# Performance work log

Hardware: AMD Instinct MI355X
Metric: run time of the kernel (lower is better)

The kernel has to match this reference:

```python
import jax, jax.numpy as jnp
import numpy as np

B, T, C, H = 4, 2048, 1024, 16
D = C // H  # head dim = 64


def setup_inputs() -> dict:
    key = jax.random.key(0)
    ks = jax.random.split(key, 6)
    s = 1.0 / np.sqrt(C)
    return {
        "x": jax.random.normal(ks[0], (B, T, C), dtype=jnp.float32),
        "Wk": jax.random.uniform(ks[1], (C, C), jnp.float32, -s, s),
        "Wq": jax.random.uniform(ks[2], (C, C), jnp.float32, -s, s),
        "Wv": jax.random.uniform(ks[3], (C, C), jnp.float32, -s, s),
        "Wp": jax.random.uniform(ks[4], (C, C), jnp.float32, -s, s),
        "bp": jax.random.uniform(ks[5], (C,), jnp.float32, -s, s),
    }


def reference(x, Wk, Wq, Wv, Wp, bp):
    # nn.Linear applies y = x @ W.T
    def split_heads(y):  # [B,T,C] -> [B,H,T,D]
        return y.reshape(B, T, H, D).transpose(0, 2, 1, 3)

    k = split_heads(x @ Wk.T)
    q = split_heads(x @ Wq.T)
    v = split_heads(x @ Wv.T)
    scale = 1.0 / np.sqrt(D)
    aff = jnp.einsum("bhtd,bhsd->bhts", q, k) * scale  # [B,H,T,T]
    aff = jax.nn.softmax(aff, axis=-1)
    out = jnp.einsum("bhts,bhsd->bhtd", aff, v)  # [B,H,T,D]
    out = out.transpose(0, 2, 1, 3).reshape(B, T, C)
    return out @ Wp.T + bp
```

## Files before the change

kernel.cpp:

```cpp
#include <hip/hip_runtime.h>
#include <stdint.h>

typedef __bf16 bf16_t;
typedef bf16_t bf16x2 __attribute__((ext_vector_type(2)));
typedef bf16_t bf16x8 __attribute__((ext_vector_type(8)));
typedef float f32x4 __attribute__((ext_vector_type(4)));
typedef float f32x16 __attribute__((ext_vector_type(16)));
typedef unsigned short u16;
typedef u16 u16x8 __attribute__((ext_vector_type(8)));
typedef u16 u16x4 __attribute__((ext_vector_type(4)));
typedef unsigned int u32;
typedef u32 u32x2 __attribute__((ext_vector_type(2)));
typedef u32 u32x4v __attribute__((ext_vector_type(4)));

__device__ __forceinline__ u16 f2b(float f) {
  uint32_t u = __builtin_bit_cast(uint32_t, f);
  u += 0x7fffu + ((u >> 16) & 1u);
  return (u16)(u >> 16);
}

__device__ __forceinline__ u32 pkbf(float lo, float hi) {
  bf16x2 t = {(__bf16)lo, (__bf16)hi};
  return __builtin_bit_cast(u32, t);
}

__device__ __forceinline__ void gl_lds16(const void* g, void* l) {
  __builtin_amdgcn_global_load_lds(
      (const __attribute__((address_space(1))) uint32_t*)(uintptr_t)g,
      (__attribute__((address_space(3))) uint32_t*)(uintptr_t)l, 16, 0, 0);
}

__global__ void cast_bf16(const float* __restrict__ src, u16* __restrict__ dst, int n8) {
  int i = blockIdx.x * blockDim.x + threadIdx.x;
  int stride = gridDim.x * blockDim.x;
  for (; i < n8; i += stride) {
    float4 a = ((const float4*)src)[2 * i];
    float4 b = ((const float4*)src)[2 * i + 1];
    u16x8 o;
    o[0] = f2b(a.x); o[1] = f2b(a.y); o[2] = f2b(a.z); o[3] = f2b(a.w);
    o[4] = f2b(b.x); o[5] = f2b(b.y); o[6] = f2b(b.z); o[7] = f2b(b.w);
    ((u16x8*)dst)[i] = o;
  }
}

__global__ void cast4_bf16(const float* __restrict__ a, const float* __restrict__ b,
                           const float* __restrict__ c, const float* __restrict__ d,
                           u16* __restrict__ dst, int n8) {
  const float* srcs[4] = {a, b, c, d};
  const float* src = srcs[blockIdx.y];
  u16* dp = dst + (size_t)blockIdx.y * (size_t)n8 * 8;
  int i = blockIdx.x * blockDim.x + threadIdx.x;
  int stride = gridDim.x * blockDim.x;
  for (; i < n8; i += stride) {
    float4 x = ((const float4*)src)[2 * i];
    float4 y = ((const float4*)src)[2 * i + 1];
    u16x8 o;
    o[0] = f2b(x.x); o[1] = f2b(x.y); o[2] = f2b(x.z); o[3] = f2b(x.w);
    o[4] = f2b(y.x); o[5] = f2b(y.y); o[6] = f2b(y.z); o[7] = f2b(y.w);
    ((u16x8*)dp)[i] = o;
  }
}

template <int MODE>
__global__ __launch_bounds__(256, 2)
void gemm_bt(const u16* __restrict__ A, const u16* __restrict__ Wt,
             u16* __restrict__ outb, float* __restrict__ outf,
             const float* __restrict__ bias, float scale) {
  __shared__ u16 As[128 * 32];
  __shared__ u16 Bs[128 * 32];
  const int tid  = threadIdx.x;
  const int lane = tid & 63;
  const int w    = tid >> 6;
  const int wm   = w >> 1, wn = w & 1;
  const int g    = lane >> 4, c = lane & 15;
  const int m0   = blockIdx.y * 128, n0 = blockIdx.x * 128;

  f32x4 acc[4][4] = {};

  const u16* gA = A  + (size_t)(m0 + w * 16 + (lane >> 2)) * 1024 + (lane & 3) * 8;
  const u16* gB = Wt + (size_t)(n0 + w * 16 + (lane >> 2)) * 1024 + (lane & 3) * 8;
  char* lA = (char*)As + w * 1024;
  char* lB = (char*)Bs + w * 1024;

#pragma unroll 1
  for (int kt = 0; kt < 1024; kt += 32) {
    __syncthreads();
    gl_lds16(gA + kt,             lA);
    gl_lds16(gA + kt + 64 * 1024, lA + 4096);
    gl_lds16(gB + kt,             lB);
    gl_lds16(gB + kt + 64 * 1024, lB + 4096);
    __syncthreads();
    bf16x8 af[4], bfr[4];
#pragma unroll
    for (int mi = 0; mi < 4; ++mi)
      af[mi] = *(const bf16x8*)&As[(wm * 64 + mi * 16 + c) * 32 + g * 8];
#pragma unroll
    for (int ni = 0; ni < 4; ++ni)
      bfr[ni] = *(const bf16x8*)&Bs[(wn * 64 + ni * 16 + c) * 32 + g * 8];
#pragma unroll
    for (int mi = 0; mi < 4; ++mi)
#pragma unroll
      for (int ni = 0; ni < 4; ++ni)
        acc[mi][ni] = __builtin_amdgcn_mfma_f32_16x16x32_bf16(af[mi], bfr[ni], acc[mi][ni], 0, 0, 0);
  }

  const int rowb = m0 + wm * 64;
  const int colb = n0 + wn * 64;

  if (MODE == 0) {
#pragma unroll
    for (int mi = 0; mi < 4; ++mi)
#pragma unroll
      for (int ni = 0; ni < 4; ++ni) {
        size_t base = (size_t)(rowb + mi * 16 + g * 4) * 1024 + (colb + ni * 16 + c);
#pragma unroll
        for (int r = 0; r < 4; ++r)
          outb[base + (size_t)r * 1024] = f2b(acc[mi][ni][r] * scale);
      }
  } else if (MODE == 1) {
#pragma unroll
    for (int mi = 0; mi < 4; ++mi) {
      int row = rowb + mi * 16 + g * 4;
      int bb = row >> 11, tl = row & 2047;
#pragma unroll
      for (int ni = 0; ni < 4; ++ni) {
        int col = colb + ni * 16 + c;
        u16x4 pk;
#pragma unroll
        for (int r = 0; r < 4; ++r) pk[r] = f2b(acc[mi][ni][r]);
        *(u16x4*)(outb + ((size_t)(bb * 1024 + col)) * 2048 + tl) = pk;
      }
    }
  } else {
#pragma unroll
    for (int ni = 0; ni < 4; ++ni) {
      int col = colb + ni * 16 + c;
      float bv = bias[col];
#pragma unroll
      for (int mi = 0; mi < 4; ++mi) {
        size_t base = (size_t)(rowb + mi * 16 + g * 4) * 1024 + col;
#pragma unroll
        for (int r = 0; r < 4; ++r)
          outf[base + (size_t)r * 1024] = acc[mi][ni][r] + bv;
      }
    }
  }
}

__global__ __launch_bounds__(256, 2)
void attn_fused(const u16* __restrict__ qb, const u16* __restrict__ kb,
                const u16* __restrict__ vt, u16* __restrict__ ob) {
  __shared__ u16 KV[2][4096];

  const int bh = blockIdx.x;
  const int qt = blockIdx.y;
  const int b  = bh >> 4, h = bh & 15;
  const int tid  = threadIdx.x;
  const int lane = tid & 63;
  const int w    = tid >> 6;
  const int l31  = lane & 31, g32 = lane >> 5;

  const int r  = tid >> 3, sl = tid & 7;
  const u16* kgp = kb + (size_t)(b * 2048 + r) * 1024 + h * 64 + sl * 8;
  const u16* vgp = vt + (size_t)(bh * 64 + r) * 2048 + sl * 8;
  const int wb = r * 128 + ((sl * 16) ^ ((r & 7) << 4));
  char* lK = (char*)&KV[0][0];
  char* lV = (char*)&KV[1][0];

  const int qrow0 = b * 2048 + qt * 256 + w * 64;
  bf16x8 qf[2][4];
#pragma unroll
  for (int q2 = 0; q2 < 2; ++q2)
#pragma unroll
    for (int dc = 0; dc < 4; ++dc)
      qf[q2][dc] = *(const bf16x8*)(qb + (size_t)(qrow0 + q2 * 32 + l31) * 1024 +
                                    h * 64 + dc * 16 + g32 * 8);

  f32x16 Oa[2][2] = {};
  float lp[2] = {0.f, 0.f};

  const int xorv = (l31 & 7) << 4;
  const int rowb = l31 * 128;

  uint4 pK0 = *(const uint4*)(kgp);
  uint4 pK1 = *(const uint4*)(kgp + (size_t)32 * 1024);
  uint4 pV0 = *(const uint4*)(vgp);
  uint4 pV1 = *(const uint4*)(vgp + (size_t)32 * 2048);

#pragma unroll 1
  for (int step = 0; step < 32; ++step) {
    __syncthreads();
    *(uint4*)(lK + wb)        = pK0;
    *(uint4*)(lK + wb + 4096) = pK1;
    *(uint4*)(lV + wb)        = pV0;
    *(uint4*)(lV + wb + 4096) = pV1;
    __syncthreads();

    if (step + 1 < 32) {
      const int s1 = (step + 1) * 64;
      pK0 = *(const uint4*)(kgp + (size_t)s1 * 1024);
      pK1 = *(const uint4*)(kgp + (size_t)(s1 + 32) * 1024);
      pV0 = *(const uint4*)(vgp + s1);
      pV1 = *(const uint4*)(vgp + s1 + (size_t)32 * 2048);
    }

    const char* kt  = (const char*)&KV[0][0];
    const char* vtl = (const char*)&KV[1][0];

#pragma unroll
    for (int kb2 = 0; kb2 < 2; ++kb2) {
      bf16x8 kf[4];
#pragma unroll
      for (int dc = 0; dc < 4; ++dc)
        kf[dc] = *(const bf16x8*)(kt + kb2 * 4096 + rowb + ((dc * 32 + g32 * 16) ^ xorv));
      bf16x8 vf[2][2];
#pragma unroll
      for (int db = 0; db < 2; ++db)
#pragma unroll
        for (int ck = 0; ck < 2; ++ck)
          vf[db][ck] = *(const bf16x8*)(vtl + db * 4096 + rowb +
                                        (((kb2 * 2 + ck) * 32 + g32 * 16) ^ xorv));

#pragma unroll
      for (int q2 = 0; q2 < 2; ++q2) {
        f32x16 S = {};
#pragma unroll
        for (int dc = 0; dc < 4; ++dc)
          S = __builtin_amdgcn_mfma_f32_32x32x16_bf16(kf[dc], qf[q2][dc], S, 0, 0, 0);

        float p[16];
#pragma unroll
        for (int rr = 0; rr < 16; ++rr) p[rr] = __builtin_amdgcn_exp2f(S[rr]);
        float s01 = (p[0] + p[1]) + (p[2] + p[3]);
        float s02 = (p[4] + p[5]) + (p[6] + p[7]);
        float s03 = (p[8] + p[9]) + (p[10] + p[11]);
        float s04 = (p[12] + p[13]) + (p[14] + p[15]);
        lp[q2] += (s01 + s02) + (s03 + s04);

        u32 w0 = pkbf(p[0], p[1]),   w1 = pkbf(p[2], p[3]);
        u32 w2 = pkbf(p[4], p[5]),   w3 = pkbf(p[6], p[7]);
        u32 w4 = pkbf(p[8], p[9]),   w5 = pkbf(p[10], p[11]);
        u32 w6 = pkbf(p[12], p[13]), w7 = pkbf(p[14], p[15]);
        u32x2 sA = __builtin_amdgcn_permlane32_swap(w0, w2, false, false);
        u32x2 sB = __builtin_amdgcn_permlane32_swap(w1, w3, false, false);
        u32x2 sC = __builtin_amdgcn_permlane32_swap(w4, w6, false, false);
        u32x2 sD = __builtin_amdgcn_permlane32_swap(w5, w7, false, false);
        u32x4v q0 = {sA[0], sB[0], sA[1], sB[1]};
        u32x4v q1 = {sC[0], sD[0], sC[1], sD[1]};
        bf16x8 pb0 = __builtin_bit_cast(bf16x8, q0);
        bf16x8 pb1 = __builtin_bit_cast(bf16x8, q1);

#pragma unroll
        for (int db = 0; db < 2; ++db) {
          Oa[q2][db] = __builtin_amdgcn_mfma_f32_32x32x16_bf16(vf[db][0], pb0, Oa[q2][db], 0, 0, 0);
          Oa[q2][db] = __builtin_amdgcn_mfma_f32_32x32x16_bf16(vf[db][1], pb1, Oa[q2][db], 0, 0, 0);
        }
      }
    }
  }

#pragma unroll
  for (int q2 = 0; q2 < 2; ++q2) {
    float v = lp[q2];
    v += __shfl_xor(v, 32);
    float rinv = 1.0f / v;
    const size_t rb = (size_t)(qrow0 + q2 * 32 + l31) * 1024 + h * 64;
#pragma unroll
    for (int db = 0; db < 2; ++db)
#pragma unroll
      for (int pr = 0; pr < 8; ++pr) {
        int reg = 2 * pr;
        int d0  = (reg & 3) + 8 * (reg >> 2) + 4 * g32 + db * 32;
        u32 pk = pkbf(Oa[q2][db][reg] * rinv, Oa[q2][db][reg + 1] * rinv);
        *(u32*)(ob + rb + d0) = pk;
      }
  }
}

extern "C" void kernel_launch(void* const* d_in, const int* in_sizes, int n_in,
                              void* d_out, int out_size, void* d_ws, size_t ws_size,
                              hipStream_t stream) {
  const float* x  = (const float*)d_in[0];
  const float* Wk = (const float*)d_in[1];
  const float* Wq = (const float*)d_in[2];
  const float* Wv = (const float*)d_in[3];
  const float* Wp = (const float*)d_in[4];
  const float* bp = (const float*)d_in[5];
  float* out = (float*)d_out;

  const size_t MC = (size_t)8192 * 1024;
  u16* xb  = (u16*)d_ws;
  u16* qb  = xb + MC;
  u16* kb2 = qb + MC;
  u16* vtb = kb2 + MC;
  u16* wqb = vtb + MC;
  u16* wkb = wqb + (size_t)1024 * 1024;
  u16* wvb = wkb + (size_t)1024 * 1024;
  u16* wpb = wvb + (size_t)1024 * 1024;
  u16* ob  = xb;

  cast_bf16<<<2048, 256, 0, stream>>>(x, xb, (int)(MC / 8));
  cast4_bf16<<<dim3(256, 4), 256, 0, stream>>>(Wq, Wk, Wv, Wp, wqb, 1024 * 1024 / 8);

  const float qscale = 0.125f * 1.44269504088896340736f;
  dim3 gg(8, 64);
  gemm_bt<0><<<gg, 256, 0, stream>>>(xb, wqb, qb,  nullptr, nullptr, qscale);
  gemm_bt<0><<<gg, 256, 0, stream>>>(xb, wkb, kb2, nullptr, nullptr, 1.0f);
  gemm_bt<1><<<gg, 256, 0, stream>>>(xb, wvb, vtb, nullptr, nullptr, 1.0f);

  attn_fused<<<dim3(64, 8), 256, 0, stream>>>(qb, kb2, vtb, ob);

  gemm_bt<2><<<gg, 256, 0, stream>>>(ob, wpb, nullptr, out, bp, 1.0f);
}
```

Baseline: 206.9 us.

## Fuse Q/K/V projections into one GEMM launch and double the K-tile depth

Replaces three separate projection GEMM launches with one kernel over a 24x64 grid, where blockIdx.x picks which weight (Q, K, V) to use and which epilogue to run. The 1536 blocks in a single launch fill the device better than three 512-block waves, and launch gaps disappear. Both GEMMs also move from a 32-wide to a 64-wide K tile per LDS stage, halving the number of barrier pairs per K sweep at the cost of twice the shared memory per block (32 KB). The larger LDS footprint and the row-stride-64 layout may add bank conflicts or reduce occupancy.

Result: faster. 183.7 us (-11.2%).

```diff
diff --git a/kernel.cpp b/kernel.cpp
--- a/kernel.cpp
+++ b/kernel.cpp
@@ -61,13 +61,92 @@
   }
 }
 
-template <int MODE>
 __global__ __launch_bounds__(256, 2)
-void gemm_bt(const u16* __restrict__ A, const u16* __restrict__ Wt,
-             u16* __restrict__ outb, float* __restrict__ outf,
-             const float* __restrict__ bias, float scale) {
-  __shared__ u16 As[128 * 32];
-  __shared__ u16 Bs[128 * 32];
+void gemm_qkv(const u16* __restrict__ A, const u16* __restrict__ W3,
+              u16* __restrict__ qb, u16* __restrict__ kb2, u16* __restrict__ vtb,
+              float qscale) {
+  __shared__ u16 As[128 * 64];
+  __shared__ u16 Bs[128 * 64];
+  const int tid  = threadIdx.x;
+  const int lane = tid & 63;
+  const int w    = tid >> 6;
+  const int wm   = w >> 1, wn = w & 1;
+  const int g    = lane >> 4, c = lane & 15;
+  const int which = blockIdx.x >> 3;
+  const int n0    = (blockIdx.x & 7) * 128;
+  const int m0    = blockIdx.y * 128;
+  const u16* Wt = W3 + (size_t)which * 1024 * 1024;
+
+  f32x4 acc[4][4] = {};
+
+  const u16* gA = A  + (size_t)(m0 + (tid >> 3)) * 1024 + (tid & 7) * 8;
+  const u16* gB = Wt + (size_t)(n0 + (tid >> 3)) * 1024 + (tid & 7) * 8;
+  char* lA = (char*)As + w * 1024;
+  char* lB = (char*)Bs + w * 1024;
+
+#pragma unroll 1
+  for (int kt = 0; kt < 1024; kt += 64) {
+    __syncthreads();
+#pragma unroll
+    for (int j = 0; j < 4; ++j) {
+      gl_lds16(gA + kt + (size_t)j * 32 * 1024, lA + j * 4096);
+      gl_lds16(gB + kt + (size_t)j * 32 * 1024, lB + j * 4096);
+    }
+    __syncthreads();
+#pragma unroll
+    for (int ks = 0; ks < 2; ++ks) {
+      bf16x8 af[4], bfr[4];
+#pragma unroll
+      for (int mi = 0; mi < 4; ++mi)
+        af[mi] = *(const bf16x8*)&As[(wm * 64 + mi * 16 + c) * 64 + ks * 32 + g * 8];
+#pragma unroll
+      for (int ni = 0; ni < 4; ++ni)
+        bfr[ni] = *(const bf16x8*)&Bs[(wn * 64 + ni * 16 + c) * 64 + ks * 32 + g * 8];
+#pragma unroll
+      for (int mi = 0; mi < 4; ++mi)
+#pragma unroll
+        for (int ni = 0; ni < 4; ++ni)
+          acc[mi][ni] = __builtin_amdgcn_mfma_f32_16x16x32_bf16(af[mi], bfr[ni], acc[mi][ni], 0, 0, 0);
+    }
+  }
+
+  const int rowb = m0 + wm * 64;
+  const int colb = n0 + wn * 64;
+
+  if (which <= 1) {
+    u16* outb = (which == 0) ? qb : kb2;
+    const float scale = (which == 0) ? qscale : 1.0f;
+#pragma unroll
+    for (int mi = 0; mi < 4; ++mi)
+#pragma unroll
+      for (int ni = 0; ni < 4; ++ni) {
+        size_t base = (size_t)(rowb + mi * 16 + g * 4) * 1024 + (colb + ni * 16 + c);
+#pragma unroll
+        for (int r = 0; r < 4; ++r)
+          outb[base + (size_t)r * 1024] = f2b(acc[mi][ni][r] * scale);
+      }
+  } else {
+#pragma unroll
+    for (int mi = 0; mi < 4; ++mi) {
+      int row = rowb + mi * 16 + g * 4;
+      int bb = row >> 11, tl = row & 2047;
+#pragma unroll
+      for (int ni = 0; ni < 4; ++ni) {
+        int col = colb + ni * 16 + c;
+        u16x4 pk;
+#pragma unroll
+        for (int r = 0; r < 4; ++r) pk[r] = f2b(acc[mi][ni][r]);
+        *(u16x4*)(vtb + ((size_t)(bb * 1024 + col)) * 2048 + tl) = pk;
+      }
+    }
+  }
+}
+
+__global__ __launch_bounds__(256, 2)
+void gemm_out(const u16* __restrict__ A, const u16* __restrict__ Wt,
+              float* __restrict__ outf, const float* __restrict__ bias) {
+  __shared__ u16 As[128 * 64];
+  __shared__ u16 Bs[128 * 64];
   const int tid  = threadIdx.x;
   const int lane = tid & 63;
   const int w    = tid >> 6;
@@ -77,72 +156,49 @@
 
   f32x4 acc[4][4] = {};
 
-  const u16* gA = A  + (size_t)(m0 + w * 16 + (lane >> 2)) * 1024 + (lane & 3) * 8;
-  const u16* gB = Wt + (size_t)(n0 + w * 16 + (lane >> 2)) * 1024 + (lane & 3) * 8;
+  const u16* gA = A  + (size_t)(m0 + (tid >> 3)) * 1024 + (tid & 7) * 8;
+  const u16* gB = Wt + (size_t)(n0 + (tid >> 3)) * 1024 + (tid & 7) * 8;
   char* lA = (char*)As + w * 1024;
   char* lB = (char*)Bs + w * 1024;
 
 #pragma unroll 1
-  for (int kt = 0; kt < 1024; kt += 32) {
-    __syncthreads();
-    gl_lds16(gA + kt,             lA);
-    gl_lds16(gA + kt + 64 * 1024, lA + 4096);
-    gl_lds16(gB + kt,             lB);
-    gl_lds16(gB + kt + 64 * 1024, lB + 4096);
-    __syncthreads();
-    bf16x8 af[4], bfr[4];
-#pragma unroll
-    for (int mi = 0; mi < 4; ++mi)
-      af[mi] = *(const bf16x8*)&As[(wm * 64 + mi * 16 + c) * 32 + g * 8];
-#pragma unroll
-    for (int ni = 0; ni < 4; ++ni)
-      bfr[ni] = *(const bf16x8*)&Bs[(wn * 64 + ni * 16 + c) * 32 + g * 8];
-#pragma unroll
-    for (int mi = 0; mi < 4; ++mi)
+  for (int kt = 0; kt < 1024; kt += 64) {
+    __syncthreads();
+#pragma unroll
+    for (int j = 0; j < 4; ++j) {
+      gl_lds16(gA + kt + (size_t)j * 32 * 1024, lA + j * 4096);
+      gl_lds16(gB + kt + (size_t)j * 32 * 1024, lB + j * 4096);
+    }
+    __syncthreads();
+#pragma unroll
+    for (int ks = 0; ks < 2; ++ks) {
+      bf16x8 af[4], bfr[4];
+#pragma unroll
+      for (int mi = 0; mi < 4; ++mi)
+        af[mi] = *(const bf16x8*)&As[(wm * 64 + mi * 16 + c) * 64 + ks * 32 + g * 8];
 #pragma unroll
       for (int ni = 0; ni < 4; ++ni)
-        acc[mi][ni] = __builtin_amdgcn_mfma_f32_16x16x32_bf16(af[mi], bfr[ni], acc[mi][ni], 0, 0, 0);
+        bfr[ni] = *(const bf16x8*)&Bs[(wn * 64 + ni * 16 + c) * 64 + ks * 32 + g * 8];
+#pragma unroll
+      for (int mi = 0; mi < 4; ++mi)
+#pragma unroll
+        for (int ni = 0; ni < 4; ++ni)
+          acc[mi][ni] = __builtin_amdgcn_mfma_f32_16x16x32_bf16(af[mi], bfr[ni], acc[mi][ni], 0, 0, 0);
+    }
   }
 
   const int rowb = m0 + wm * 64;
   const int colb = n0 + wn * 64;
-
-  if (MODE == 0) {
-#pragma unroll
-    for (int mi = 0; mi < 4; ++mi)
-#pragma unroll
-      for (int ni = 0; ni < 4; ++ni) {
-        size_t base = (size_t)(rowb + mi * 16 + g * 4) * 1024 + (colb + ni * 16 + c);
-#pragma unroll
-        for (int r = 0; r < 4; ++r)
-          outb[base + (size_t)r * 1024] = f2b(acc[mi][ni][r] * scale);
-      }
-  } else if (MODE == 1) {
+#pragma unroll
+  for (int ni = 0; ni < 4; ++ni) {
+    int col = colb + ni * 16 + c;
+    float bv = bias[col];
 #pragma unroll
     for (int mi = 0; mi < 4; ++mi) {
-      int row = rowb + mi * 16 + g * 4;
-      int bb = row >> 11, tl = row & 2047;
-#pragma unroll
-      for (int ni = 0; ni < 4; ++ni) {
-        int col = colb + ni * 16 + c;
-        u16x4 pk;
-#pragma unroll
-        for (int r = 0; r < 4; ++r) pk[r] = f2b(acc[mi][ni][r]);
-        *(u16x4*)(outb + ((size_t)(bb * 1024 + col)) * 2048 + tl) = pk;
-      }
-    }
-  } else {
-#pragma unroll
-    for (int ni = 0; ni < 4; ++ni) {
-      int col = colb + ni * 16 + c;
-      float bv = bias[col];
-#pragma unroll
-      for (int mi = 0; mi < 4; ++mi) {
-        size_t base = (size_t)(rowb + mi * 16 + g * 4) * 1024 + col;
-#pragma unroll
-        for (int r = 0; r < 4; ++r)
-          outf[base + (size_t)r * 1024] = acc[mi][ni][r] + bv;
-      }
+      size_t base = (size_t)(rowb + mi * 16 + g * 4) * 1024 + col;
+#pragma unroll
+      for (int r = 0; r < 4; ++r)
+        outf[base + (size_t)r * 1024] = acc[mi][ni][r] + bv;
     }
   }
 }
@@ -294,21 +350,16 @@
   u16* kb2 = qb + MC;
   u16* vtb = kb2 + MC;
   u16* wqb = vtb + MC;
-  u16* wkb = wqb + (size_t)1024 * 1024;
-  u16* wvb = wkb + (size_t)1024 * 1024;
-  u16* wpb = wvb + (size_t)1024 * 1024;
+  u16* wpb = wqb + (size_t)3 * 1024 * 1024;
   u16* ob  = xb;
 
   cast_bf16<<<2048, 256, 0, stream>>>(x, xb, (int)(MC / 8));
   cast4_bf16<<<dim3(256, 4), 256, 0, stream>>>(Wq, Wk, Wv, Wp, wqb, 1024 * 1024 / 8);
 
   const float qscale = 0.125f * 1.44269504088896340736f;
-  dim3 gg(8, 64);
-  gemm_bt<0><<<gg, 256, 0, stream>>>(xb, wqb, qb,  nullptr, nullptr, qscale);
-  gemm_bt<0><<<gg, 256, 0, stream>>>(xb, wkb, kb2, nullptr, nullptr, 1.0f);
-  gemm_bt<1><<<gg, 256, 0, stream>>>(xb, wvb, vtb, nullptr, nullptr, 1.0f);
+  gemm_qkv<<<dim3(24, 64), 256, 0, stream>>>(xb, wqb, qb, kb2, vtb, qscale);
 
   attn_fused<<<dim3(64, 8), 256, 0, stream>>>(qb, kb2, vtb, ob);
 
-  gemm_bt<2><<<gg, 256, 0, stream>>>(ob, wpb, nullptr, out, bp, 1.0f);
-}
+  gemm_out<<<dim3(8, 64), 256, 0, stream>>>(ob, wpb, out, bp);
+}
```
